# Kernel tuning notes

Measured on AMD Instinct MI355X. Metric: run time of the kernel, lower is better.

## Reference

```python
import jax, jax.numpy as jnp
import numpy as np
import math

MAX_DEGREE = 8  # n_harmonics = (MAX_DEGREE+1)**2 = 81


def _real_sph_harm_all(theta, phi, L):
    """Real part of scipy's sph_harm(m, l, phi, theta) for all (l, m),
    l in [0, L], m in [-l, l], stacked on the last axis (81 terms for L=8).

    Uses the stable associated-Legendre recurrence (with Condon-Shortley
    phase, matching scipy) instead of a per-term CPU loop.
    """
    x = jnp.cos(theta)
    s = jnp.sin(theta)  # sin(theta) >= 0 since theta in [0, pi]

    # P[(l, m)] = associated Legendre P_l^m(cos theta), 0 <= m <= l <= L
    P = {}
    for m in range(L + 1):
        if m == 0:
            Pmm = jnp.ones_like(x)
        else:
            # P_m^m = -(2m-1) * sin(theta) * P_{m-1}^{m-1}  (Condon-Shortley)
            Pmm = -(2 * m - 1) * s * P[(m - 1, m - 1)]
        P[(m, m)] = Pmm
        if m + 1 <= L:
            P[(m + 1, m)] = (2 * m + 1) * x * Pmm
        for l in range(m + 2, L + 1):
            P[(l, m)] = ((2 * l - 1) * x * P[(l - 1, m)]
                         - (l + m - 1) * P[(l - 2, m)]) / (l - m)

    ys = []
    for l in range(L + 1):
        for m in range(-l, l + 1):
            am = abs(m)
            norm = math.sqrt((2 * l + 1) / (4.0 * math.pi)
                             * math.factorial(l - am) / math.factorial(l + am))
            # Re(Y_l^m) = N * P_l^{|m|}(cos th) * cos(|m| phi); for m<0 multiply
            # by (-1)^{|m|} since Y_l^{-m} = (-1)^m conj(Y_l^m) (scipy convention).
            Y = norm * P[(l, am)] * jnp.cos(am * phi)
            if m < 0:
                Y = Y * ((-1.0) ** am)
            ys.append(Y)
    return jnp.stack(ys, axis=-1)  # [batch, channels, (L+1)^2]


def setup_inputs() -> dict:
    key = jax.random.key(0)
    k1, k2 = jax.random.split(key)
    positions = jax.random.normal(k1, (32, 1024, 3), dtype=jnp.float32)
    harmonics_weights = jax.random.normal(k2, (81, 2048), dtype=jnp.float32)
    return {"positions": positions, "harmonics_weights": harmonics_weights}


def reference(positions, harmonics_weights):
    # normalize to unit sphere
    r = jnp.linalg.norm(positions, axis=-1, keepdims=True)
    pos = positions / (r + 1e-8)
    theta = jnp.arccos(jnp.clip(pos[..., 2], -1.0, 1.0))  # polar angle
    phi = jnp.arctan2(pos[..., 1], pos[..., 0])           # azimuth
    harmonics = _real_sph_harm_all(theta, phi, MAX_DEGREE)  # [B, C, 81]
    return jnp.matmul(harmonics, harmonics_weights)         # [B, C, 2048]
```

## Files before the change

kernel.cpp:

```cpp
#include <hip/hip_runtime.h>


typedef __attribute__((ext_vector_type(8))) short bf16x8;
typedef __attribute__((ext_vector_type(4))) float f32x4;

#define BM 128
#define BN 128
#define LDA 104
#define KPAD 96
#define LDCC 132

constexpr double PI_D = 3.14159265358979323846;
constexpr double csqrt_c(double v) {
  if (v <= 0.0) return 0.0;
  double g = v < 1.0 ? 1.0 : v;
  for (int i = 0; i < 100; ++i) g = 0.5 * (g + v / g);
  return g;
}
struct Norms { float c[81]; };
constexpr Norms make_norms() {
  Norms n{};
  for (int l = 0; l <= 8; ++l)
    for (int m = -l; m <= l; ++m) {
      int am = m < 0 ? -m : m;
      double fr = 1.0;
      for (int i = l - am + 1; i <= l + am; ++i) fr *= (double)i;
      double v = csqrt_c((2.0 * l + 1.0) / (4.0 * PI_D) / fr);
      if (m < 0 && (am & 1)) v = -v;
      n.c[l * l + l + m] = (float)v;
    }
  return n;
}
constexpr Norms NORMS = make_norms();

__device__ __forceinline__ unsigned f2bf(float f) {
  unsigned u = __float_as_uint(f);
  return (u + 0x7fffu + ((u >> 16) & 1u)) >> 16;
}

__global__ __launch_bounds__(256)
void wt_convert_kernel(const float* __restrict__ W, unsigned short* __restrict__ WT, int nch) {
  const int t = blockIdx.x * 256 + threadIdx.x;
  if (t >= nch * 12) return;
  const int kg = t / nch;
  const int c  = t - kg * nch;
  unsigned short v[8];
#pragma unroll
  for (int j = 0; j < 8; ++j) {
    const int k = kg * 8 + j;
    v[j] = (k < 81) ? (unsigned short)f2bf(W[(size_t)k * nch + c]) : (unsigned short)0;
  }
  unsigned* dst = reinterpret_cast<unsigned*>(WT + (size_t)c * KPAD + kg * 8);
#pragma unroll
  for (int j = 0; j < 4; ++j)
    dst[j] = (unsigned)v[2 * j] | ((unsigned)v[2 * j + 1] << 16);
}

__global__ __launch_bounds__(256)
void sph_mfma_kernel(const float* __restrict__ pos,
                     const unsigned short* __restrict__ WT,
                     float* __restrict__ out, int nch)
{
  __shared__ __align__(16) char smem[64 * LDCC * 4];
  unsigned short* H = reinterpret_cast<unsigned short*>(smem);
  float*          C = reinterpret_cast<float*>(smem);

  const int tid  = threadIdx.x;
  const int lane = tid & 63;
  const int wid  = tid >> 6;
  const int wc   = wid >> 1, wp = wid & 1;
  const int l15  = lane & 15, l4 = lane >> 4;
  const int mblk = blockIdx.y, nblk = blockIdx.x;

  if (tid < BM) {
    const int gp = mblk * BM + tid;
    const float px = pos[gp * 3 + 0];
    const float py = pos[gp * 3 + 1];
    const float pz = pos[gp * 3 + 2];
    const float r   = sqrtf(px * px + py * py + pz * pz);
    const float inv = 1.0f / (r + 1e-8f);
    const float xn = px * inv, yn = py * inv, zn = pz * inv;
    const float x = fminf(1.0f, fmaxf(-1.0f, zn));
    const float s = sqrtf(fmaxf(0.0f, 1.0f - x * x));
    const float rho = sqrtf(xn * xn + yn * yn);
    const float c1  = rho > 0.0f ? xn / rho : 1.0f;

    float cm[9];
    cm[0] = 1.0f; cm[1] = c1;
#pragma unroll
    for (int m = 2; m <= 8; ++m) cm[m] = 2.0f * c1 * cm[m - 1] - cm[m - 2];

    unsigned short* hrow = &H[tid * LDA];
    float Pmm_prev = 1.0f;
#pragma unroll
    for (int m = 0; m <= 8; ++m) {
      const float Pmm = (m == 0) ? 1.0f : -(float)(2 * m - 1) * s * Pmm_prev;
      Pmm_prev = Pmm;
      {
        const float base = Pmm * cm[m];
        hrow[m * m + 2 * m] = (unsigned short)f2bf(NORMS.c[m * m + 2 * m] * base);
        if (m > 0)
          hrow[m * m] = (unsigned short)f2bf(NORMS.c[m * m] * base);
      }
      float Pl2 = Pmm, Pl1 = 0.0f;
      if (m + 1 <= 8) {
        Pl1 = (float)(2 * m + 1) * x * Pmm;
        const int l = m + 1;
        const float base = Pl1 * cm[m];
        hrow[l * l + l + m] = (unsigned short)f2bf(NORMS.c[l * l + l + m] * base);
        if (m > 0)
          hrow[l * l + l - m] = (unsigned short)f2bf(NORMS.c[l * l + l - m] * base);
      }
#pragma unroll
      for (int l = m + 2; l <= 8; ++l) {
        const float Pl = ((float)(2 * l - 1) * x * Pl1
                          - (float)(l + m - 1) * Pl2) * (1.0f / (float)(l - m));
        Pl2 = Pl1; Pl1 = Pl;
        const float base = Pl * cm[m];
        hrow[l * l + l + m] = (unsigned short)f2bf(NORMS.c[l * l + l + m] * base);
        if (m > 0)
          hrow[l * l + l - m] = (unsigned short)f2bf(NORMS.c[l * l + l - m] * base);
      }
    }
#pragma unroll
    for (int i = 81; i < KPAD; ++i) hrow[i] = 0;
  }

  __syncthreads();

  const unsigned short* wt_base =
      WT + (size_t)(nblk * BN + wc * 64 + l15) * KPAD + l4 * 8;
  f32x4 acc[4][4] = {};
#pragma unroll
  for (int kk = 0; kk < 3; ++kk) {
    bf16x8 wfrag[4], hfrag[4];
#pragma unroll
    for (int i = 0; i < 4; ++i)
      wfrag[i] = *reinterpret_cast<const bf16x8*>(
          wt_base + (size_t)i * 16 * KPAD + kk * 32);
#pragma unroll
    for (int i = 0; i < 4; ++i)
      hfrag[i] = *reinterpret_cast<const bf16x8*>(
          &H[(wp * 64 + i * 16 + l15) * LDA + kk * 32 + l4 * 8]);
#pragma unroll
    for (int cmr = 0; cmr < 4; ++cmr)
#pragma unroll
      for (int pn = 0; pn < 4; ++pn)
        acc[cmr][pn] = __builtin_amdgcn_mfma_f32_16x16x32_bf16(
            wfrag[cmr], hfrag[pn], acc[cmr][pn], 0, 0, 0);
  }

  __syncthreads();

  const size_t obase = (size_t)(mblk * BM) * nch + (size_t)nblk * BN;
#pragma unroll
  for (int h = 0; h < 2; ++h) {
#pragma unroll
    for (int q = 0; q < 2; ++q) {
      const int lr = wp * 32 + q * 16 + l15;
#pragma unroll
      for (int cmr = 0; cmr < 4; ++cmr)
        *reinterpret_cast<f32x4*>(&C[lr * LDCC + wc * 64 + cmr * 16 + l4 * 4]) =
            acc[cmr][2 * h + q];
    }
    __syncthreads();
#pragma unroll
    for (int it = 0; it < 8; ++it) {
      const int f  = it * 1024 + tid * 4;
      const int lr = f >> 7;
      const int cc = f & 127;
      const int gr = (lr >> 5) * 64 + h * 32 + (lr & 31);
      const f32x4 v = *reinterpret_cast<const f32x4*>(&C[lr * LDCC + cc]);
      *reinterpret_cast<f32x4*>(out + obase + (size_t)gr * nch + cc) = v;
    }
    if (h == 0) __syncthreads();
  }
}

extern "C" void kernel_launch(void* const* d_in, const int* in_sizes, int n_in,
                              void* d_out, int out_size, void* d_ws, size_t ws_size,
                              hipStream_t stream) {
  const float* pos = (const float*)d_in[0];
  const float* W   = (const float*)d_in[1];
  float*       out = (float*)d_out;
  const int npts = in_sizes[0] / 3;
  const int nch  = in_sizes[1] / 81;

  unsigned short* WT = (unsigned short*)d_ws;
  wt_convert_kernel<<<(nch * 12 + 255) / 256, 256, 0, stream>>>(W, WT, nch);
  dim3 grid(nch / BN, npts / BM);
  sph_mfma_kernel<<<grid, 256, 0, stream>>>(pos, WT, out, nch);
}
```

Baseline: 56.73 us.

## Fuse weight bf16 conversion into main kernel via shared-memory staging

Removes the separate weight-transpose/convert kernel and its launch. Each block now loads its 81x128 fp32 weight band directly, converts it to bf16 and stores it transposed into shared memory, and MFMA fragments are read from LDS instead of a global workspace. This drops one kernel launch and the global round trip of the converted weights. In exchange every one of the 256 blocks along the point dimension redoes the conversion, shared memory grows, and the transposed LDS stores are scattered 2-byte writes that may cause bank conflicts.

```diff
diff --git a/kernel.cpp b/kernel.cpp
--- a/kernel.cpp
+++ b/kernel.cpp
@@ -39,31 +39,14 @@
 }
 
 __global__ __launch_bounds__(256)
-void wt_convert_kernel(const float* __restrict__ W, unsigned short* __restrict__ WT, int nch) {
-  const int t = blockIdx.x * 256 + threadIdx.x;
-  if (t >= nch * 12) return;
-  const int kg = t / nch;
-  const int c  = t - kg * nch;
-  unsigned short v[8];
-#pragma unroll
-  for (int j = 0; j < 8; ++j) {
-    const int k = kg * 8 + j;
-    v[j] = (k < 81) ? (unsigned short)f2bf(W[(size_t)k * nch + c]) : (unsigned short)0;
-  }
-  unsigned* dst = reinterpret_cast<unsigned*>(WT + (size_t)c * KPAD + kg * 8);
-#pragma unroll
-  for (int j = 0; j < 4; ++j)
-    dst[j] = (unsigned)v[2 * j] | ((unsigned)v[2 * j + 1] << 16);
-}
-
-__global__ __launch_bounds__(256)
 void sph_mfma_kernel(const float* __restrict__ pos,
-                     const unsigned short* __restrict__ WT,
+                     const float* __restrict__ W,
                      float* __restrict__ out, int nch)
 {
-  __shared__ __align__(16) char smem[64 * LDCC * 4];
-  unsigned short* H = reinterpret_cast<unsigned short*>(smem);
-  float*          C = reinterpret_cast<float*>(smem);
+  __shared__ __align__(16) char smem[2 * BM * LDA * 2];
+  unsigned short* H  = reinterpret_cast<unsigned short*>(smem);
+  unsigned short* Wl = reinterpret_cast<unsigned short*>(smem + BM * LDA * 2);
+  float*          C  = reinterpret_cast<float*>(smem);
 
   const int tid  = threadIdx.x;
   const int lane = tid & 63;
@@ -71,6 +54,25 @@
   const int wc   = wid >> 1, wp = wid & 1;
   const int l15  = lane & 15, l4 = lane >> 4;
   const int mblk = blockIdx.y, nblk = blockIdx.x;
+
+  {
+    const float* wband = W + (size_t)nblk * BN;
+    for (int idx = tid; idx < 81 * (BN / 4); idx += 256) {
+      const int k  = idx / (BN / 4);
+      const int c4 = idx - k * (BN / 4);
+      const float4 w = *reinterpret_cast<const float4*>(
+          wband + (size_t)k * nch + c4 * 4);
+      unsigned short* col = &Wl[(c4 * 4) * LDA + k];
+      col[0 * LDA] = (unsigned short)f2bf(w.x);
+      col[1 * LDA] = (unsigned short)f2bf(w.y);
+      col[2 * LDA] = (unsigned short)f2bf(w.z);
+      col[3 * LDA] = (unsigned short)f2bf(w.w);
+    }
+    if (tid < BM) {
+#pragma unroll
+      for (int i = 81; i < KPAD; ++i) Wl[tid * LDA + i] = 0;
+    }
+  }
 
   if (tid < BM) {
     const int gp = mblk * BM + tid;
@@ -128,8 +130,6 @@
 
   __syncthreads();
 
-  const unsigned short* wt_base =
-      WT + (size_t)(nblk * BN + wc * 64 + l15) * KPAD + l4 * 8;
   f32x4 acc[4][4] = {};
 #pragma unroll
   for (int kk = 0; kk < 3; ++kk) {
@@ -137,7 +137,7 @@
 #pragma unroll
     for (int i = 0; i < 4; ++i)
       wfrag[i] = *reinterpret_cast<const bf16x8*>(
-          wt_base + (size_t)i * 16 * KPAD + kk * 32);
+          &Wl[(wc * 64 + i * 16 + l15) * LDA + kk * 32 + l4 * 8]);
 #pragma unroll
     for (int i = 0; i < 4; ++i)
       hfrag[i] = *reinterpret_cast<const bf16x8*>(
@@ -186,8 +186,6 @@
   const int npts = in_sizes[0] / 3;
   const int nch  = in_sizes[1] / 81;
 
-  unsigned short* WT = (unsigned short*)d_ws;
-  wt_convert_kernel<<<(nch * 12 + 255) / 256, 256, 0, stream>>>(W, WT, nch);
   dim3 grid(nch / BN, npts / BM);
-  sph_mfma_kernel<<<grid, 256, 0, stream>>>(pos, WT, out, nch);
+  sph_mfma_kernel<<<grid, 256, 0, stream>>>(pos, W, out, nch);
 }
```

Measured after the change: 76.23 us. 1.34x slower.
